# Optimization experiments

Hardware: AMD Instinct MI355X
Metric: run time of the kernel (lower is better)

Reference implementation:

```python
import jax, jax.numpy as jnp
import numpy as np
import math

SI, VI = 128, 32
H_DIM = 32          # max(vi, vo) for q/k/v GVPs; max(vi, 0)=32 for weight_proj
HEADS = 4
N_ANCHORS = 32
S_H, V_H = SI // HEADS, VI // HEADS  # 32, 8


def _norm_no_nan(x, axis=-1, keepdims=False, eps=1e-8):
    return jnp.sqrt(jnp.maximum(jnp.sum(x * x, axis=axis, keepdims=keepdims), eps))


def _gvp_full(s, v, wh, ws_w, ws_b, wv, wsv_w, wsv_b):
    # GVP with activations=(silu, sigmoid), vector_gate=True, vo>0
    vt = jnp.swapaxes(v, -1, -2)                 # [..., 3, vi]
    vh = vt @ wh.T                               # [..., 3, h]
    vn = _norm_no_nan(vh, axis=-2)               # [..., h]
    s_out = jnp.concatenate([s, vn], -1) @ ws_w.T + ws_b   # [..., so]
    v_out = jnp.swapaxes(vh @ wv.T, -1, -2)      # [..., vo, 3]
    gate = jax.nn.sigmoid(s_out) @ wsv_w.T + wsv_b
    v_out = v_out * jax.nn.sigmoid(gate)[..., None]
    return jax.nn.silu(s_out), v_out


def _gvp_scalar(s, v, wh, ws_w, ws_b):
    # weight_proj: activations=(None, None), vo=0 -> scalar output only
    vt = jnp.swapaxes(v, -1, -2)
    vh = vt @ wh.T
    vn = _norm_no_nan(vh, axis=-2)
    return jnp.concatenate([s, vn], -1) @ ws_w.T + ws_b


def setup_inputs() -> dict:
    key = jax.random.key(0)
    ks = jax.random.split(key, 32)
    N, C = 8192, 16
    inp = {
        's': jax.random.normal(ks[0], (N, C, SI), jnp.float32),
        'v': jax.random.normal(ks[1], (N, C, VI, 3), jnp.float32),
    }

    def lin(k, out_d, in_d):
        return jax.random.normal(k, (out_d, in_d), jnp.float32) / math.sqrt(in_d)

    # weight_proj: GVP((128,32) -> (32,0)), h_dim = max(32,0) = 32
    inp['wp_wh'] = lin(ks[2], H_DIM, VI)
    inp['wp_ws_w'] = lin(ks[3], N_ANCHORS, H_DIM + SI)
    inp['wp_ws_b'] = jnp.zeros((N_ANCHORS,), jnp.float32)
    # to_q / to_k / to_v: GVP((128,32) -> (128,32)), h_dim = 32
    i = 4
    for p in ('q', 'k', 'vp'):
        inp[f'{p}_wh'] = lin(ks[i], H_DIM, VI); i += 1
        inp[f'{p}_ws_w'] = lin(ks[i], SI, H_DIM + SI); i += 1
        inp[f'{p}_ws_b'] = jnp.zeros((SI,), jnp.float32)
        inp[f'{p}_wv'] = lin(ks[i], VI, H_DIM); i += 1
        inp[f'{p}_wsv_w'] = lin(ks[i], VI, SI); i += 1
        inp[f'{p}_wsv_b'] = jnp.zeros((VI,), jnp.float32)
    return inp


def reference(s, v, wp_wh, wp_ws_w, wp_ws_b,
              q_wh, q_ws_w, q_ws_b, q_wv, q_wsv_w, q_wsv_b,
              k_wh, k_ws_w, k_ws_b, k_wv, k_wsv_w, k_wsv_b,
              vp_wh, vp_ws_w, vp_ws_b, vp_wv, vp_wsv_w, vp_wsv_b):
    N, C = s.shape[:2]
    H, r = HEADS, N_ANCHORS

    # Compress: softmax over nodes -> r anchors
    p_logits = _gvp_scalar(s, v, wp_wh, wp_ws_w, wp_ws_b)       # [N, C, r]
    p_weights = jax.nn.softmax(p_logits, axis=0)
    s_global = jnp.einsum('nca,ncs->acs', p_weights, s)          # [r, C, si]
    v_global = jnp.einsum('nca,ncvd->acvd', p_weights, v)        # [r, C, vi, 3]

    s_q, v_q = _gvp_full(s, v, q_wh, q_ws_w, q_ws_b, q_wv, q_wsv_w, q_wsv_b)
    s_k, v_k = _gvp_full(s_global, v_global, k_wh, k_ws_w, k_ws_b, k_wv, k_wsv_w, k_wsv_b)
    s_val, v_val = _gvp_full(s_global, v_global, vp_wh, vp_ws_w, vp_ws_b, vp_wv, vp_wsv_w, vp_wsv_b)

    # split heads
    qs = s_q.reshape(N, C, H, S_H); qv = v_q.reshape(N, C, H, V_H, 3)
    ks_ = s_k.reshape(r, C, H, S_H); kv = v_k.reshape(r, C, H, V_H, 3)
    vs = s_val.reshape(r, C, H, S_H); vv = v_val.reshape(r, C, H, V_H, 3)

    s_dot = jnp.einsum('nchs,rchs->nrch', qs, ks_)
    v_dot = jnp.einsum('nchvd,rchvd->nrch', qv, kv)
    energy = (s_dot + v_dot) / math.sqrt(S_H + V_H)
    alpha = jax.nn.softmax(energy, axis=1)                       # softmax over anchors r
    # dropout is identity at inference

    out_s = jnp.einsum('nrch,rchs->nchs', alpha, vs).reshape(N, C, SI)
    out_v = jnp.einsum('nrch,rchvd->nchvd', alpha, vv).reshape(N, C, VI, 3)
    return out_s, out_v
```

## Files before the change

### kernel.cpp

```cpp
#include <hip/hip_runtime.h>
#include <stdint.h>

typedef unsigned short ushort_t;
typedef __attribute__((ext_vector_type(8))) short short8;
typedef __attribute__((ext_vector_type(4))) float float4v;

static constexpr int N_=8192, C_=16;

static constexpr long OFF_LOGITS = 0;
static constexpr long OFF_PM  = 4194304;
static constexpr long OFF_PS  = 4210688;
static constexpr long OFF_M   = 4227072;
static constexpr long OFF_INV = 4227584;
static constexpr long OFF_SGL = 4228096;
static constexpr long OFF_VGL = 4293632;
static constexpr long OFF_KATT= 4342784;
static constexpr long OFF_VATT= 4408320;
static constexpr long OFF_WF  = 4473856;
static constexpr long WF_WHQ=0, WF_WHWP=1024, WF_KWH=2048, WF_KWS=3072, WF_KWV=23552,
  WF_KWSV=24576, WF_VWH=28672, WF_VWS=29696, WF_VWV=50176, WF_VWSV=51200,
  WF_B1=55296 , WF_BG=70656 ,
  WF_BV=72704 ;

static constexpr long VH_B   = 67108864;
static constexpr long AVN_B  = 92274688;

__device__ __forceinline__ uint32_t f2bf(float f){
  uint32_t u = __float_as_uint(f);
  return (u + 0x7FFFu + ((u>>16)&1u)) >> 16;
}

__device__ __forceinline__ long katt_idx(int c, int h, int k, int r){
  int kt=k>>5, kk=k&31, nt=r>>4;
  int lane=((kk>>3)<<4)|(r&15), j=kk&7;
  return ((((long)(c*4+h)*2+kt)*2+nt)*64+lane)*8+j;
}
__device__ __forceinline__ long vatt_idx(int c, int h, int r, int n2){
  int nt=n2>>4;
  int lane=((r>>3)<<4)|(n2&15), j=r&7;
  return (((long)(c*4+h)*4+nt)*64+lane)*8+j;
}

__global__ void k0_prep(const float* __restrict__ wpwh, const float* __restrict__ wpws,
    const float* __restrict__ qwh, const float* __restrict__ qws, const float* __restrict__ qwv,
    const float* __restrict__ qwsv, const float* __restrict__ kwh, const float* __restrict__ kws,
    const float* __restrict__ kwv, const float* __restrict__ kwsv, const float* __restrict__ vwh,
    const float* __restrict__ vws, const float* __restrict__ vwv, const float* __restrict__ vwsv,
    float* __restrict__ wsf){
  int job=blockIdx.x, t=threadIdx.x;
  float* W = wsf + OFF_WF;
  auto tr=[&](const float* src, float* dst, int O, int J){
    for(int idx=t; idx<O*J; idx+=blockDim.x){int o=idx/J, j=idx-o*J; dst[j*O+o]=src[idx];}
  };
  switch(job){
    case 0: tr(qwh,  W+WF_WHQ, 32,32); break;
    case 1: tr(wpwh, W+WF_WHWP,32,32); break;
    case 2: tr(kwh,  W+WF_KWH, 32,32); break;
    case 3: tr(kws,  W+WF_KWS, 128,160); break;
    case 4: tr(kwv,  W+WF_KWV, 32,32); break;
    case 5: tr(kwsv, W+WF_KWSV,32,128); break;
    case 6: tr(vwh,  W+WF_VWH, 32,32); break;
    case 7: tr(vws,  W+WF_VWS, 128,160); break;
    case 8: tr(vwv,  W+WF_VWV, 32,32); break;
    case 9: tr(vwsv, W+WF_VWSV,32,128); break;
    case 10: {
      ushort_t* dst=(ushort_t*)(W+WF_B1);
      for(int idx=t; idx<30720; idx+=blockDim.x){
        int j=idx&7, lane=(idx>>3)&63, tn=idx>>9, nt=tn%10, kt=tn/10;
        int k=kt*32+((lane>>4)<<3)+j, n=nt*16+(lane&15);
        float val;
        if(k<128)       val = (n<128)? qws[n*160+k]            : wpws[(n-128)*160+k];
        else if(k<160)  val = (n<128)? qws[n*160+k]            : 0.f;
        else            val = (n<128)? 0.f                     : wpws[(n-128)*160+(k-32)];
        dst[idx]=(ushort_t)f2bf(val);
      } } break;
    case 11: {
      ushort_t* dst=(ushort_t*)(W+WF_BG);
      for(int idx=t; idx<4096; idx+=blockDim.x){
        int j=idx&7, lane=(idx>>3)&63, tn=idx>>9, nt=tn&1, kt=tn>>1;
        int k=kt*32+((lane>>4)<<3)+j, n=nt*16+(lane&15);
        dst[idx]=(ushort_t)f2bf(qwsv[n*128+k]);
      } } break;
    case 12: {
      ushort_t* dst=(ushort_t*)(W+WF_BV);
      for(int idx=t; idx<1024; idx+=blockDim.x){
        int j=idx&7, lane=(idx>>3)&63, nt=idx>>9;
        int k=((lane>>4)<<3)+j, n=nt*16+(lane&15);
        dst[idx]=(ushort_t)f2bf(qwv[n*32+k]);
      } } break;
  }
}

__global__ __launch_bounds__(256) void kA_vn(const float* __restrict__ v,
    const float* __restrict__ wsf, ushort_t* __restrict__ vh_s, ushort_t* __restrict__ avn_s){
  __shared__ float whq[1024], whwp[1024];
  __shared__ float vb[4][96];
  int t=threadIdx.x, wave=t>>6, lane=t&63;
  for(int i=t;i<1024;i+=256){ whq[i]=wsf[OFF_WF+WF_WHQ+i]; whwp[i]=wsf[OFF_WF+WF_WHWP+i]; }
  __syncthreads();
  int h=lane&31, half=lane>>5;
  for(int it=0; it<32; it++){
    long inst = ((long)blockIdx.x*4 + wave)*32 + it;
    if(lane<48) ((float2*)vb[wave])[lane] = ((const float2*)v)[inst*48+lane];
    float d0=0,d1=0,d2=0;
    for(int i=half*16;i<half*16+16;i++){ float w=whq[i*32+h];
      d0+=vb[wave][3*i]*w; d1+=vb[wave][3*i+1]*w; d2+=vb[wave][3*i+2]*w; }
    d0+=__shfl_xor(d0,32,64); d1+=__shfl_xor(d1,32,64); d2+=__shfl_xor(d2,32,64);
    if(lane<32){
      float vn=sqrtf(fmaxf(d0*d0+d1*d1+d2*d2,1e-8f));
      avn_s[inst*64+h]=(ushort_t)f2bf(vn);
      vh_s[(inst*3+0)*32+h]=(ushort_t)f2bf(d0);
      vh_s[(inst*3+1)*32+h]=(ushort_t)f2bf(d1);
      vh_s[(inst*3+2)*32+h]=(ushort_t)f2bf(d2);
    }
    float e0=0,e1=0,e2=0;
    for(int i=half*16;i<half*16+16;i++){ float w=whwp[i*32+h];
      e0+=vb[wave][3*i]*w; e1+=vb[wave][3*i+1]*w; e2+=vb[wave][3*i+2]*w; }
    e0+=__shfl_xor(e0,32,64); e1+=__shfl_xor(e1,32,64); e2+=__shfl_xor(e2,32,64);
    if(lane<32){
      float vn=sqrtf(fmaxf(e0*e0+e1*e1+e2*e2,1e-8f));
      avn_s[inst*64+32+h]=(ushort_t)f2bf(vn);
    }
  }
}

__global__ __launch_bounds__(256) void kB_gemm(const float* __restrict__ s,
    float* __restrict__ wsf,
    const float* __restrict__ qwsb, const float* __restrict__ wpwsb,
    const float* __restrict__ qwsvb,
    ushort_t* __restrict__ qatt, const ushort_t* __restrict__ vh_s,
    const ushort_t* __restrict__ avn_s){
  __shared__ ushort_t sigl[4][16*136];
  __shared__ float    gsigl[4][16*33];
  int t=threadIdx.x, wave=t>>6, lane=t&63;
  int l15=lane&15, lq=lane>>4;
  long m0 = ((long)blockIdx.x*4 + wave)*16;
  const short8* B1 = (const short8*)(wsf + OFF_WF + WF_B1);
  const short8* BG = (const short8*)(wsf + OFF_WF + WF_BG);
  const short8* BV = (const short8*)(wsf + OFF_WF + WF_BV);
  float4v acc[10];
  #pragma unroll
  for(int i=0;i<10;i++) acc[i]=(float4v){0.f,0.f,0.f,0.f};
  #pragma unroll
  for(int kt=0;kt<4;kt++){
    const float* sp = s + (m0+l15)*128 + kt*32 + lq*8;
    float4 f0=*(const float4*)sp, f1=*(const float4*)(sp+4);
    short8 a;
    a[0]=(short)f2bf(f0.x); a[1]=(short)f2bf(f0.y); a[2]=(short)f2bf(f0.z); a[3]=(short)f2bf(f0.w);
    a[4]=(short)f2bf(f1.x); a[5]=(short)f2bf(f1.y); a[6]=(short)f2bf(f1.z); a[7]=(short)f2bf(f1.w);
    #pragma unroll
    for(int nt=0;nt<10;nt++)
      acc[nt]=__builtin_amdgcn_mfma_f32_16x16x32_bf16(a, B1[(kt*10+nt)*64+lane], acc[nt],0,0,0);
  }
  #pragma unroll
  for(int kt=4;kt<6;kt++){
    short8 a = *(const short8*)&avn_s[(m0+l15)*64 + (kt-4)*32 + lq*8];
    #pragma unroll
    for(int nt=0;nt<10;nt++)
      acc[nt]=__builtin_amdgcn_mfma_f32_16x16x32_bf16(a, B1[(kt*10+nt)*64+lane], acc[nt],0,0,0);
  }
  ushort_t* sl = sigl[wave]; float* gl = gsigl[wave];
  #pragma unroll
  for(int nt=0;nt<8;nt++){
    float b = qwsb[nt*16+l15];
    #pragma unroll
    for(int reg=0;reg<4;reg++){
      float x = acc[nt][reg] + b;
      float sg = 1.f/(1.f+__expf(-x));
      int row = lq*4+reg, col=nt*16+l15;
      long inst = m0+row;
      qatt[(inst*4 + (col>>5))*64 + (col&31)] = (ushort_t)f2bf(x*sg);
      sl[row*136+col] = (ushort_t)f2bf(sg);
    }
  }
  #pragma unroll
  for(int nt=8;nt<10;nt++){
    float b = wpwsb[(nt-8)*16+l15];
    #pragma unroll
    for(int reg=0;reg<4;reg++){
      long inst=m0+lq*4+reg;
      wsf[OFF_LOGITS + inst*32 + (nt-8)*16+l15] = acc[nt][reg]+b;
    }
  }
  __syncthreads();
  float4v g0=(float4v){0.f,0.f,0.f,0.f}, g1=g0;
  #pragma unroll
  for(int kt=0;kt<4;kt++){
    short8 a = *(const short8*)&sl[l15*136 + kt*32 + lq*8];
    g0=__builtin_amdgcn_mfma_f32_16x16x32_bf16(a, BG[(kt*2+0)*64+lane], g0,0,0,0);
    g1=__builtin_amdgcn_mfma_f32_16x16x32_bf16(a, BG[(kt*2+1)*64+lane], g1,0,0,0);
  }
  {
    float b0 = qwsvb[l15], b1 = qwsvb[16+l15];
    #pragma unroll
    for(int reg=0;reg<4;reg++){
      int row=lq*4+reg;
      gl[row*33 + l15]    = 1.f/(1.f+__expf(-(g0[reg]+b0)));
      gl[row*33 + 16+l15] = 1.f/(1.f+__expf(-(g1[reg]+b1)));
    }
  }
  __syncthreads();
  #pragma unroll
  for(int tt=0;tt<3;tt++){
    short8 a = *(const short8*)&vh_s[(m0*3 + tt*16 + l15)*32 + lq*8];
    float4v v0=(float4v){0.f,0.f,0.f,0.f}, v1=v0;
    v0=__builtin_amdgcn_mfma_f32_16x16x32_bf16(a, BV[0*64+lane], v0,0,0,0);
    v1=__builtin_amdgcn_mfma_f32_16x16x32_bf16(a, BV[1*64+lane], v1,0,0,0);
    #pragma unroll
    for(int nt2=0;nt2<2;nt2++){
      #pragma unroll
      for(int reg=0;reg<4;reg++){
        int lr = tt*16 + lq*4 + reg;
        int il = lr/3, d = lr - il*3;
        int o = nt2*16+l15;
        float val = (nt2? v1[reg] : v0[reg]) * gl[il*33+o];
        long inst = m0 + il;
        qatt[(inst*4 + (o>>3))*64 + 32 + (o&7)*3 + d] = (ushort_t)f2bf(val);
      }
    }
  }
}

__global__ __launch_bounds__(256) void k2a_stats(float* __restrict__ ws){
  int c = blockIdx.x; int chunk = blockIdx.y;
  int t=threadIdx.x; int i=t>>5, a=t&31;
  const float* L = ws + OFF_LOGITS;
  float m=-1e30f, sum=0.f;
  for(int k2=0;k2<32;k2++){
    int n = chunk*256 + k2*8 + i;
    float x = L[((long)n*16 + c)*32 + a];
    float mn = fmaxf(m,x);
    sum = sum*__expf(m-mn) + __expf(x-mn);
    m = mn;
  }
  __shared__ float sm[8][32], ss[8][32];
  sm[i][a]=m; ss[i][a]=sum;
  __syncthreads();
  if(t<32){
    float M=sm[0][t], S=ss[0][t];
    for(int q=1;q<8;q++){
      float mq=sm[q][t], sq_=ss[q][t];
      float mn=fmaxf(M,mq); S=S*__expf(M-mn)+sq_*__expf(mq-mn); M=mn;
    }
    ws[OFF_PM + (chunk*16+c)*32 + t]=M;
    ws[OFF_PS + (chunk*16+c)*32 + t]=S;
  }
}

__global__ __launch_bounds__(256) void k2b_merge(float* __restrict__ ws){
  int t = blockIdx.x*256 + threadIdx.x;
  if(t>=512) return;
  int c=t>>5, a=t&31;
  float M=-1e30f, S=0.f;
  for(int ch=0; ch<32; ch++){
    float mq=ws[OFF_PM+(ch*16+c)*32+a], sq_=ws[OFF_PS+(ch*16+c)*32+a];
    float mn=fmaxf(M,mq); S=S*__expf(M-mn)+sq_*__expf(mq-mn); M=mn;
  }
  ws[OFF_M + t]=M; ws[OFF_INV + t]=1.0f/S;
}

__global__ __launch_bounds__(256) void k3_globals(const float* __restrict__ s,
    const float* __restrict__ v, float* __restrict__ ws){
  int c = blockIdx.x & 15; int chunk = blockIdx.x >> 4;
  int t=threadIdx.x; int wave=t>>6, lane=t&63;
  float M=0.f, INV=0.f;
  if(lane<32){ M=ws[OFF_M+c*32+lane]; INV=ws[OFF_INV+c*32+lane]; }
  float4 acc[32];
  #pragma unroll
  for(int a2=0;a2<32;a2++) acc[a2]=make_float4(0.f,0.f,0.f,0.f);
  const float4* s4=(const float4*)s; const float4* v4=(const float4*)v;
  const float* L = ws+OFF_LOGITS;
  for(int it=0; it<64; it++){
    int n = chunk*256 + it*4 + wave;
    long inst = (long)n*16 + c;
    float4 x = make_float4(0.f,0.f,0.f,0.f);
    float w = 0.f;
    if(lane<32){ x = s4[inst*32+lane]; w = __expf(L[inst*32+lane] - M)*INV; }
    else if(lane<56){ x = v4[inst*24 + (lane-32)]; }
    #pragma unroll
    for(int a2=0;a2<32;a2++){
      float wa = __shfl(w, a2, 64);
      acc[a2].x += wa*x.x; acc[a2].y += wa*x.y; acc[a2].z += wa*x.z; acc[a2].w += wa*x.w;
    }
  }
  __shared__ float sacc[32][228];
  float* sf = &sacc[0][0];
  for(int idx=t; idx<32*228; idx+=256) sf[idx]=0.f;
  __syncthreads();
  if(lane<56){
    int db = (lane<32)? lane*4 : 128 + (lane-32)*4;
    #pragma unroll
    for(int a2=0;a2<32;a2++){
      atomicAdd(&sacc[a2][db+0], acc[a2].x);
      atomicAdd(&sacc[a2][db+1], acc[a2].y);
      atomicAdd(&sacc[a2][db+2], acc[a2].z);
      atomicAdd(&sacc[a2][db+3], acc[a2].w);
    }
  }
  __syncthreads();
  for(int idx=t; idx<32*224; idx+=256){
    int a2=idx/224, d=idx-a2*224;
    float val = sacc[a2][d];
    if(d<128) atomicAdd(&ws[OFF_SGL + ((long)a2*16+c)*128 + d], val);
    else      atomicAdd(&ws[OFF_VGL + ((long)a2*16+c)*96 + (d-128)], val);
  }
}

__global__ __launch_bounds__(64) void k4_kvgvp(float* __restrict__ wsf,
    const float* __restrict__ k_wsb, const float* __restrict__ k_wsvb,
    const float* __restrict__ v_wsb, const float* __restrict__ v_wsvb){
  int a = blockIdx.x >> 4, c = blockIdx.x & 15;
  int lane = threadIdx.x;
  __shared__ __align__(16) float cat[160];
  __shared__ __align__(16) float vb2[96];
  __shared__ float vhb[96];
  __shared__ __align__(16) float sg[128];
  const float* W = wsf + OFF_WF;
  ushort_t* katt = (ushort_t*)(wsf + OFF_KATT);
  ushort_t* vatt = (ushort_t*)(wsf + OFF_VATT);
  long inst = (long)a*16 + c;
  ((float2*)cat)[lane] = ((const float2*)(wsf+OFF_SGL))[inst*64 + lane];
  if(lane<48) ((float2*)vb2)[lane] = ((const float2*)(wsf+OFF_VGL))[inst*48 + lane];
  __syncthreads();
  if(a==0){
    for(int idx=lane; idx<1024; idx+=64){
      int h2=idx&3, kk=56+((idx>>2)&7), r=idx>>5;
      katt[katt_idx(c,h2,kk,r)]=0;
      vatt[vatt_idx(c,h2,r,kk)]=0;
    }
  }
  int h = lane&31, half = lane>>5;
  for(int p=0;p<2;p++){
    const float* wht  = W + (p? WF_VWH  : WF_KWH);
    const float* wst  = W + (p? WF_VWS  : WF_KWS);
    const float* wvt  = W + (p? WF_VWV  : WF_KWV);
    const float* wsvt = W + (p? WF_VWSV : WF_KWSV);
    const float* bs   = p? v_wsb : k_wsb;
    const float* bsv  = p? v_wsvb : k_wsvb;
    float d0=0.f,d1=0.f,d2=0.f;
    for(int i=half*16; i<half*16+16; i++){
      float w_=wht[i*32+h];
      d0+=vb2[3*i]*w_; d1+=vb2[3*i+1]*w_; d2+=vb2[3*i+2]*w_;
    }
    d0 += __shfl_xor(d0,32,64); d1 += __shfl_xor(d1,32,64); d2 += __shfl_xor(d2,32,64);
    if(lane<32){
      cat[128+h] = sqrtf(fmaxf(d0*d0+d1*d1+d2*d2, 1e-8f));
      vhb[3*h]=d0; vhb[3*h+1]=d1; vhb[3*h+2]=d2;
    }
    __syncthreads();
    float a0=bs[lane], a1=bs[lane+64];
    for(int j=0;j<160;j+=4){
      float4 c4=*((float4*)&cat[j]);
      a0 += c4.x*wst[j*128+lane]      + c4.y*wst[(j+1)*128+lane]
          + c4.z*wst[(j+2)*128+lane]  + c4.w*wst[(j+3)*128+lane];
      a1 += c4.x*wst[j*128+64+lane]   + c4.y*wst[(j+1)*128+64+lane]
          + c4.z*wst[(j+2)*128+64+lane]+ c4.w*wst[(j+3)*128+64+lane];
    }
    float sig0=1.f/(1.f+__expf(-a0)), sig1=1.f/(1.f+__expf(-a1));
    float silu0=a0*sig0, silu1=a1*sig1;
    sg[lane]=sig0; sg[lane+64]=sig1;
    {
      int o=lane, hh2=o>>5, k=o&31;
      if(p==0) katt[katt_idx(c,hh2,k,a)] = (ushort_t)f2bf(silu0);
      else     vatt[vatt_idx(c,hh2,a,k)] = (ushort_t)f2bf(silu0);
    }
    {
      int o=lane+64, hh2=o>>5, k=o&31;
      if(p==0) katt[katt_idx(c,hh2,k,a)] = (ushort_t)f2bf(silu1);
      else     vatt[vatt_idx(c,hh2,a,k)] = (ushort_t)f2bf(silu1);
    }
    __syncthreads();
    float gacc=0.f;
    for(int o=half*64; o<half*64+64; o+=4){
      float4 s4_=*((float4*)&sg[o]);
      gacc += s4_.x*wsvt[o*32+h]+s4_.y*wsvt[(o+1)*32+h]+s4_.z*wsvt[(o+2)*32+h]+s4_.w*wsvt[(o+3)*32+h];
    }
    gacc += __shfl_xor(gacc,32,64);
    float sgate = 1.f/(1.f+__expf(-(gacc + bsv[h])));
    float e0=0.f,e1=0.f,e2=0.f;
    for(int hh=half*16; hh<half*16+16; hh++){
      float w_=wvt[hh*32+h];
      e0+=vhb[3*hh]*w_; e1+=vhb[3*hh+1]*w_; e2+=vhb[3*hh+2]*w_;
    }
    e0+=__shfl_xor(e0,32,64); e1+=__shfl_xor(e1,32,64); e2+=__shfl_xor(e2,32,64);
    if(lane<32){
      int hh2=lane>>3, oo=lane&7;
      float vals[3]={e0*sgate, e1*sgate, e2*sgate};
      #pragma unroll
      for(int d=0;d<3;d++){
        if(p==0) katt[katt_idx(c,hh2,32+oo*3+d,a)] = (ushort_t)f2bf(vals[d]);
        else     vatt[vatt_idx(c,hh2,a,32+oo*3+d)] = (ushort_t)f2bf(vals[d]);
      }
    }
    __syncthreads();
  }
}

__global__ __launch_bounds__(256) void k5_attn(const float* __restrict__ wsf, float* out){
  __shared__ ushort_t al[4][4*16*40];
  int t=threadIdx.x, wave=t>>6, lane=t&63;
  int l15=lane&15, lq=lane>>4;
  int c=blockIdx.y;
  long n0 = ((long)blockIdx.x*4+wave)*16;
  const ushort_t* qatt = (const ushort_t*)out;
  const short8* KA = (const short8*)(wsf + OFF_KATT);
  const short8* VA = (const short8*)(wsf + OFF_VATT);
  const float scale = 0.15811388300841897f;
  float4v e[4][2];
  #pragma unroll
  for(int h=0;h<4;h++){ e[h][0]=(float4v){0.f,0.f,0.f,0.f}; e[h][1]=e[h][0]; }
  #pragma unroll
  for(int h=0;h<4;h++){
    #pragma unroll
    for(int kt=0;kt<2;kt++){
      short8 a = *(const short8*)&qatt[(((n0+l15)*16 + c)*4 + h)*64 + kt*32 + lq*8];
      e[h][0]=__builtin_amdgcn_mfma_f32_16x16x32_bf16(a, KA[(((c*4+h)*2+kt)*2+0)*64+lane], e[h][0],0,0,0);
      e[h][1]=__builtin_amdgcn_mfma_f32_16x16x32_bf16(a, KA[(((c*4+h)*2+kt)*2+1)*64+lane], e[h][1],0,0,0);
    }
  }
  ushort_t* alw = al[wave];
  #pragma unroll
  for(int h=0;h<4;h++){
    #pragma unroll
    for(int reg=0;reg<4;reg++){
      float a0=e[h][0][reg]*scale, a1=e[h][1][reg]*scale;
      float m=fmaxf(a0,a1);
      m=fmaxf(m,__shfl_xor(m,1,64)); m=fmaxf(m,__shfl_xor(m,2,64));
      m=fmaxf(m,__shfl_xor(m,4,64)); m=fmaxf(m,__shfl_xor(m,8,64));
      float p0=__expf(a0-m), p1=__expf(a1-m);
      float sum=p0+p1;
      sum+=__shfl_xor(sum,1,64); sum+=__shfl_xor(sum,2,64);
      sum+=__shfl_xor(sum,4,64); sum+=__shfl_xor(sum,8,64);
      float inv=1.f/sum;
      int row=lq*4+reg;
      alw[h*640 + row*40 + l15]      = (ushort_t)f2bf(p0*inv);
      alw[h*640 + row*40 + 16 + l15] = (ushort_t)f2bf(p1*inv);
    }
  }
  __syncthreads();
  float* outv = out + 16777216;
  #pragma unroll
  for(int h=0;h<4;h++){
    short8 a = *(const short8*)&alw[h*640 + l15*40 + lq*8];
    #pragma unroll
    for(int nt=0;nt<4;nt++){
      float4v o_=(float4v){0.f,0.f,0.f,0.f};
      o_=__builtin_amdgcn_mfma_f32_16x16x32_bf16(a, VA[((c*4+h)*4+nt)*64+lane], o_,0,0,0);
      #pragma unroll
      for(int reg=0;reg<4;reg++){
        int n2=nt*16+l15, row=lq*4+reg;
        long inst=(n0+row)*16+c;
        float val=o_[reg];
        if(n2<32)      out[inst*128 + h*32+n2]=val;
        else if(n2<56) outv[inst*96 + h*24 + n2-32]=val;
      }
    }
  }
}

extern "C" void kernel_launch(void* const* d_in, const int* in_sizes, int n_in,
                              void* d_out, int out_size, void* d_ws, size_t ws_size,
                              hipStream_t stream){
  (void)in_sizes; (void)n_in; (void)out_size; (void)ws_size;
  const float* s = (const float*)d_in[0];
  const float* v = (const float*)d_in[1];
  float* wsf = (float*)d_ws;
  float* out = (float*)d_out;
  ushort_t* qatt  = (ushort_t*)d_out;
  ushort_t* vh_s  = (ushort_t*)((char*)d_out + VH_B);
  ushort_t* avn_s = (ushort_t*)((char*)d_out + AVN_B);
  (void)hipMemsetAsync((char*)d_ws + OFF_SGL*sizeof(float), 0, (size_t)(65536+49152)*sizeof(float), stream);
  k0_prep<<<13,256,0,stream>>>(
      (const float*)d_in[2],(const float*)d_in[3],
      (const float*)d_in[5],(const float*)d_in[6],(const float*)d_in[8],(const float*)d_in[9],
      (const float*)d_in[11],(const float*)d_in[12],(const float*)d_in[14],(const float*)d_in[15],
      (const float*)d_in[17],(const float*)d_in[18],(const float*)d_in[20],(const float*)d_in[21], wsf);
  kA_vn<<<1024,256,0,stream>>>(v, wsf, vh_s, avn_s);
  kB_gemm<<<2048,256,0,stream>>>(s, wsf, (const float*)d_in[7], (const float*)d_in[4],
                                 (const float*)d_in[10], qatt, vh_s, avn_s);
  k2a_stats<<<dim3(16,32),256,0,stream>>>(wsf);
  k2b_merge<<<2,256,0,stream>>>(wsf);
  k3_globals<<<512,256,0,stream>>>(s, v, wsf);
  k4_kvgvp<<<512,64,0,stream>>>(wsf, (const float*)d_in[13], (const float*)d_in[16],
                                (const float*)d_in[19], (const float*)d_in[22]);
  k5_attn<<<dim3(128,16),256,0,stream>>>(wsf, out);
}
```

Before: 592.6 us.

## Compute anchor-weighted global features with split-bf16 MFMA in k3

Rewrites the k3_globals reduction, where softmax anchor weights multiply s and v, as MFMA 16x16x32 bf16 matrix products. Each fp32 operand is split into a hi/lo bf16 pair and three products are accumulated, so precision stays close to fp32. Each wave handles a fixed slice of feature columns, and results are atomically added straight to global memory, dropping the shared-memory staging. The grid doubles to 1024 blocks of 128 rows each. The trade-off is strided scalar global loads, extra conversion arithmetic, and more global atomics.

```diff
diff --git a/kernel.cpp b/kernel.cpp
--- a/kernel.cpp
+++ b/kernel.cpp
@@ -28,6 +28,16 @@
 __device__ __forceinline__ uint32_t f2bf(float f){
   uint32_t u = __float_as_uint(f);
   return (u + 0x7FFFu + ((u>>16)&1u)) >> 16;
+}
+
+__device__ __forceinline__ void split_bf(float f, short& hi, short& lo){
+  uint32_t u = __float_as_uint(f);
+  uint32_t h = (u + 0x7FFFu + ((u>>16)&1u)) >> 16;
+  hi = (short)h;
+  float fh = __uint_as_float(h << 16);
+  float r = f - fh;
+  uint32_t u2 = __float_as_uint(r);
+  lo = (short)((u2 + 0x7FFFu + ((u2>>16)&1u)) >> 16);
 }
 
 __device__ __forceinline__ long katt_idx(int c, int h, int k, int r){
@@ -259,51 +269,75 @@
   ws[OFF_M + t]=M; ws[OFF_INV + t]=1.0f/S;
 }
 
+template<int NMT, bool ISV>
+__device__ __forceinline__ void k3_body(const float* __restrict__ X, int d0,
+    const float* __restrict__ L, float M0, float M1, float I0, float I1,
+    int c, int nb0, int l15, int lq, float* __restrict__ ws){
+  constexpr int XP = ISV ? 96 : 128;
+  float4v acc[NMT][2];
+  #pragma unroll
+  for(int mi=0;mi<NMT;mi++){
+    acc[mi][0]=(float4v){0.f,0.f,0.f,0.f};
+    acc[mi][1]=(float4v){0.f,0.f,0.f,0.f};
+  }
+  #pragma unroll
+  for(int kt=0;kt<4;kt++){
+    int nb = nb0 + kt*32 + lq*8;
+    short8 bh0, bl0, bh1, bl1;
+    #pragma unroll
+    for(int j=0;j<8;j++){
+      long ro = ((long)(nb+j)*16 + c)*32;
+      float w0 = __expf(L[ro + l15]      - M0) * I0;
+      float w1 = __expf(L[ro + 16 + l15] - M1) * I1;
+      short h_, lo_;
+      split_bf(w0, h_, lo_); bh0[j]=h_; bl0[j]=lo_;
+      split_bf(w1, h_, lo_); bh1[j]=h_; bl1[j]=lo_;
+    }
+    #pragma unroll
+    for(int mi=0;mi<NMT;mi++){
+      short8 ah, al_;
+      #pragma unroll
+      for(int j=0;j<8;j++){
+        float f = X[((long)(nb+j)*16 + c)*XP + d0 + mi*16 + l15];
+        short h_, lo_;
+        split_bf(f, h_, lo_); ah[j]=h_; al_[j]=lo_;
+      }
+      acc[mi][0]=__builtin_amdgcn_mfma_f32_16x16x32_bf16(ah,  bh0, acc[mi][0],0,0,0);
+      acc[mi][0]=__builtin_amdgcn_mfma_f32_16x16x32_bf16(al_, bh0, acc[mi][0],0,0,0);
+      acc[mi][0]=__builtin_amdgcn_mfma_f32_16x16x32_bf16(ah,  bl0, acc[mi][0],0,0,0);
+      acc[mi][1]=__builtin_amdgcn_mfma_f32_16x16x32_bf16(ah,  bh1, acc[mi][1],0,0,0);
+      acc[mi][1]=__builtin_amdgcn_mfma_f32_16x16x32_bf16(al_, bh1, acc[mi][1],0,0,0);
+      acc[mi][1]=__builtin_amdgcn_mfma_f32_16x16x32_bf16(ah,  bl1, acc[mi][1],0,0,0);
+    }
+  }
+  #pragma unroll
+  for(int mi=0;mi<NMT;mi++){
+    #pragma unroll
+    for(int nt=0;nt<2;nt++){
+      int a = nt*16 + l15;
+      #pragma unroll
+      for(int reg=0;reg<4;reg++){
+        int dloc = d0 + mi*16 + lq*4 + reg;
+        if(ISV) atomicAdd(&ws[OFF_VGL + ((long)a*16+c)*96  + dloc], acc[mi][nt][reg]);
+        else    atomicAdd(&ws[OFF_SGL + ((long)a*16+c)*128 + dloc], acc[mi][nt][reg]);
+      }
+    }
+  }
+}
+
 __global__ __launch_bounds__(256) void k3_globals(const float* __restrict__ s,
     const float* __restrict__ v, float* __restrict__ ws){
   int c = blockIdx.x & 15; int chunk = blockIdx.x >> 4;
-  int t=threadIdx.x; int wave=t>>6, lane=t&63;
-  float M=0.f, INV=0.f;
-  if(lane<32){ M=ws[OFF_M+c*32+lane]; INV=ws[OFF_INV+c*32+lane]; }
-  float4 acc[32];
-  #pragma unroll
-  for(int a2=0;a2<32;a2++) acc[a2]=make_float4(0.f,0.f,0.f,0.f);
-  const float4* s4=(const float4*)s; const float4* v4=(const float4*)v;
-  const float* L = ws+OFF_LOGITS;
-  for(int it=0; it<64; it++){
-    int n = chunk*256 + it*4 + wave;
-    long inst = (long)n*16 + c;
-    float4 x = make_float4(0.f,0.f,0.f,0.f);
-    float w = 0.f;
-    if(lane<32){ x = s4[inst*32+lane]; w = __expf(L[inst*32+lane] - M)*INV; }
-    else if(lane<56){ x = v4[inst*24 + (lane-32)]; }
-    #pragma unroll
-    for(int a2=0;a2<32;a2++){
-      float wa = __shfl(w, a2, 64);
-      acc[a2].x += wa*x.x; acc[a2].y += wa*x.y; acc[a2].z += wa*x.z; acc[a2].w += wa*x.w;
-    }
-  }
-  __shared__ float sacc[32][228];
-  float* sf = &sacc[0][0];
-  for(int idx=t; idx<32*228; idx+=256) sf[idx]=0.f;
-  __syncthreads();
-  if(lane<56){
-    int db = (lane<32)? lane*4 : 128 + (lane-32)*4;
-    #pragma unroll
-    for(int a2=0;a2<32;a2++){
-      atomicAdd(&sacc[a2][db+0], acc[a2].x);
-      atomicAdd(&sacc[a2][db+1], acc[a2].y);
-      atomicAdd(&sacc[a2][db+2], acc[a2].z);
-      atomicAdd(&sacc[a2][db+3], acc[a2].w);
-    }
-  }
-  __syncthreads();
-  for(int idx=t; idx<32*224; idx+=256){
-    int a2=idx/224, d=idx-a2*224;
-    float val = sacc[a2][d];
-    if(d<128) atomicAdd(&ws[OFF_SGL + ((long)a2*16+c)*128 + d], val);
-    else      atomicAdd(&ws[OFF_VGL + ((long)a2*16+c)*96 + (d-128)], val);
-  }
+  int t=threadIdx.x, wave=t>>6, lane=t&63;
+  int l15=lane&15, lq=lane>>4;
+  const float* L = ws + OFF_LOGITS;
+  float M0 = ws[OFF_M   + c*32 + l15],      M1 = ws[OFF_M   + c*32 + 16 + l15];
+  float I0 = ws[OFF_INV + c*32 + l15],      I1 = ws[OFF_INV + c*32 + 16 + l15];
+  int nb0 = chunk*128;
+  if(wave==0)      k3_body<4,false>(s, 0,   L, M0,M1,I0,I1, c, nb0, l15, lq, ws);
+  else if(wave==1) k3_body<4,false>(s, 64,  L, M0,M1,I0,I1, c, nb0, l15, lq, ws);
+  else if(wave==2) k3_body<3,true >(v, 0,   L, M0,M1,I0,I1, c, nb0, l15, lq, ws);
+  else             k3_body<3,true >(v, 48,  L, M0,M1,I0,I1, c, nb0, l15, lq, ws);
 }
 
 __global__ __launch_bounds__(64) void k4_kvgvp(float* __restrict__ wsf,
@@ -480,7 +514,7 @@
                                  (const float*)d_in[10], qatt, vh_s, avn_s);
   k2a_stats<<<dim3(16,32),256,0,stream>>>(wsf);
   k2b_merge<<<2,256,0,stream>>>(wsf);
-  k3_globals<<<512,256,0,stream>>>(s, v, wsf);
+  k3_globals<<<1024,256,0,stream>>>(s, v, wsf);
   k4_kvgvp<<<512,64,0,stream>>>(wsf, (const float*)d_in[13], (const float*)d_in[16],
                                 (const float*)d_in[19], (const float*)d_in[22]);
   k5_attn<<<dim3(128,16),256,0,stream>>>(wsf, out);
```

After: 583.8 us. No clear change (-1.5%).
